# Performance work log

Hardware: AMD Instinct MI355X
Metric: run time of the kernel (lower is better)

The kernel has to match this reference:

```python
import jax, jax.numpy as jnp
import numpy as np

D_MODEL = 1024
NUM_HEADS = 16
D_K = D_MODEL // NUM_HEADS  # 64
B, S = 4, 1024


def setup_inputs() -> dict:
    key = jax.random.key(0)
    ks = jax.random.split(key, 8)
    scale = 1.0 / np.sqrt(D_MODEL)
    return {
        "query": jax.random.normal(ks[0], (B, S, D_MODEL), dtype=jnp.float32),
        "key": jax.random.normal(ks[1], (B, S, D_MODEL), dtype=jnp.float32),
        "value": jax.random.normal(ks[2], (B, S, D_MODEL), dtype=jnp.float32),
        "mask": jnp.ones((B, S, S), dtype=jnp.int32),
        # per-head projection weights, stacked: [H, d_model, d_k]
        "Wq": jax.random.normal(ks[3], (NUM_HEADS, D_MODEL, D_K), dtype=jnp.float32) * scale,
        "Wk": jax.random.normal(ks[4], (NUM_HEADS, D_MODEL, D_K), dtype=jnp.float32) * scale,
        "Wv": jax.random.normal(ks[5], (NUM_HEADS, D_MODEL, D_K), dtype=jnp.float32) * scale,
        # out projection: [H*d_v, d_model]
        "Wo": jax.random.normal(ks[6], (NUM_HEADS * D_K, D_MODEL), dtype=jnp.float32) * scale,
    }


def reference(query, key, value, mask, Wq, Wk, Wv, Wo):
    H, _, d_k = Wq.shape
    b, s, _ = query.shape
    inv_sqrt_dk = 1.0 / np.sqrt(d_k).astype(np.float32)
    # per-head projections (vectorized over heads): [H, B, S, d_k]
    q = jnp.einsum("bsd,hdk->hbsk", query, Wq)
    k = jnp.einsum("bsd,hdk->hbsk", key, Wk)
    v = jnp.einsum("bsd,hdk->hbsk", value, Wv)
    # raw scores before masking are what the torch module returns as q_key_dots
    scores = jnp.einsum("hbqk,hbmk->hbqm", q, k) * inv_sqrt_dk  # [H,B,Sq,Sk]
    masked = jnp.where(mask[None, :, :, :] == 0, -jnp.inf, scores)
    p_attn = jax.nn.softmax(masked, axis=-1)
    attn_out = jnp.einsum("hbqm,hbmk->hbqk", p_attn, v)  # [H,B,S,d_k]
    # concat heads along last dim in head order (matches torch.cat over h)
    concat = jnp.transpose(attn_out, (1, 2, 0, 3)).reshape(b, s, H * d_k)
    out = concat @ Wo  # [B,S,d_model]
    # torch returns (out, list of per-head masked scores); stack as [H,B,S,S]
    return out, masked
```

## Files before the change

### kernel.cpp

```cpp
#include <hip/hip_runtime.h>
#include <hip/hip_bf16.h>
#include <math.h>

typedef __attribute__((ext_vector_type(8))) short short8;
typedef __attribute__((ext_vector_type(4))) float f32x4;


static __device__ __forceinline__ unsigned short f2bf(float x) {
  union { float f; unsigned u; } v; v.f = x;
  unsigned r = v.u + 0x7fffu + ((v.u >> 16) & 1u);
  return (unsigned short)(r >> 16);
}

__global__ __launch_bounds__(256) void proj_kernel(
    const float* __restrict__ q_in, const float* __restrict__ k_in,
    const float* __restrict__ v_in, const float* __restrict__ Wq,
    const float* __restrict__ Wk, const float* __restrict__ Wv,
    unsigned short* __restrict__ qws, unsigned short* __restrict__ kws,
    unsigned short* __restrict__ vws) {
  __shared__ unsigned short As[64 * 72];
  __shared__ unsigned short Bs[64 * 72];
  const int tid = threadIdx.x;
  const int s0 = blockIdx.x * 64;
  const int h = blockIdx.y;
  const int b = blockIdx.z & 3;
  const int which = blockIdx.z >> 2;
  const float* X = which == 0 ? q_in : (which == 1 ? k_in : v_in);
  const float* W = which == 0 ? Wq : (which == 1 ? Wk : Wv);

  const int w = tid >> 6, lane = tid & 63, q16 = lane & 15, quad = lane >> 4;

  f32x4 acc[4];
  #pragma unroll
  for (int j = 0; j < 4; ++j) acc[j] = (f32x4)0.0f;

  for (int kt = 0; kt < 16; ++kt) {
    #pragma unroll
    for (int p = 0; p < 4; ++p) {
      int idx = tid + p * 256;
      int r = idx >> 4, c4 = idx & 15;
      const float4 v = *(const float4*)(X + (size_t)(b * 1024 + s0 + r) * 1024 + kt * 64 + c4 * 4);
      ushort4 u;
      u.x = f2bf(v.x); u.y = f2bf(v.y); u.z = f2bf(v.z); u.w = f2bf(v.w);
      *(ushort4*)&As[r * 72 + c4 * 4] = u;
    }
    #pragma unroll
    for (int p = 0; p < 16; ++p) {
      int dl = p * 4 + (tid >> 6);
      int n = tid & 63;
      float wv = W[(size_t)h * 65536 + (size_t)(kt * 64 + dl) * 64 + n];
      Bs[n * 72 + dl] = f2bf(wv);
    }
    __syncthreads();
    #pragma unroll
    for (int kk = 0; kk < 2; ++kk) {
      short8 a = *(const short8*)&As[(w * 16 + q16) * 72 + kk * 32 + quad * 8];
      #pragma unroll
      for (int j = 0; j < 4; ++j) {
        short8 bb = *(const short8*)&Bs[(j * 16 + q16) * 72 + kk * 32 + quad * 8];
        acc[j] = __builtin_amdgcn_mfma_f32_16x16x32_bf16(a, bb, acc[j], 0, 0, 0);
      }
    }
    __syncthreads();
  }

  const size_t bh = (size_t)(b * 16 + h);
  #pragma unroll
  for (int j = 0; j < 4; ++j) {
    #pragma unroll
    for (int r = 0; r < 4; ++r) {
      int sl = w * 16 + quad * 4 + r;
      int ko = j * 16 + q16;
      unsigned short val = f2bf(acc[j][r]);
      if (which == 2)
        vws[(bh * 64 + ko) * 1024 + (s0 + sl)] = val;
      else if (which == 1)
        kws[(bh * 1024 + (s0 + sl)) * 64 + ko] = val;
      else
        qws[(bh * 1024 + (s0 + sl)) * 64 + ko] = val;
    }
  }
}

__global__ __launch_bounds__(256) void attn_kernel(
    const unsigned short* __restrict__ qws, const unsigned short* __restrict__ kws,
    const unsigned short* __restrict__ vws, const int* __restrict__ mask,
    float* __restrict__ scores, unsigned short* __restrict__ cws) {
  __shared__ unsigned short Qs[64 * 72];
  __shared__ unsigned short Ks[64 * 72];
  __shared__ unsigned short Vts[64 * 72];
  __shared__ unsigned short Ps[64 * 72];
  const int tid = threadIdx.x;
  const int q0 = blockIdx.x * 64;
  const int h = blockIdx.y;
  const int b = blockIdx.z;
  const int w = tid >> 6, lane = tid & 63, q16 = lane & 15, quad = lane >> 4;
  const size_t bh = (size_t)(b * 16 + h);

  {
    const unsigned short* src = qws + (bh * 1024 + q0) * 64;
    #pragma unroll
    for (int p = 0; p < 2; ++p) {
      int idx = tid + p * 256, r = idx >> 3, c = idx & 7;
      *(uint4*)&Qs[r * 72 + c * 8] = *(const uint4*)(src + r * 64 + c * 8);
    }
  }

  f32x4 o[4];
  #pragma unroll
  for (int j = 0; j < 4; ++j) o[j] = (f32x4)0.0f;
  float m_run[4] = {-3.0e38f, -3.0e38f, -3.0e38f, -3.0e38f};
  float l_run[4] = {0.f, 0.f, 0.f, 0.f};

  for (int kt = 0; kt < 16; ++kt) {
    {
      const unsigned short* ksrc = kws + (bh * 1024 + (size_t)kt * 64) * 64;
      const unsigned short* vsrc = vws + bh * 64 * 1024 + kt * 64;
      #pragma unroll
      for (int p = 0; p < 2; ++p) {
        int idx = tid + p * 256, r = idx >> 3, c = idx & 7;
        *(uint4*)&Ks[r * 72 + c * 8] = *(const uint4*)(ksrc + r * 64 + c * 8);
        *(uint4*)&Vts[r * 72 + c * 8] = *(const uint4*)(vsrc + (size_t)r * 1024 + c * 8);
      }
    }
    __syncthreads();

    f32x4 sacc[4];
    #pragma unroll
    for (int j = 0; j < 4; ++j) sacc[j] = (f32x4)0.0f;
    #pragma unroll
    for (int kk = 0; kk < 2; ++kk) {
      short8 a = *(const short8*)&Qs[(w * 16 + q16) * 72 + kk * 32 + quad * 8];
      #pragma unroll
      for (int j = 0; j < 4; ++j) {
        short8 bb = *(const short8*)&Ks[(j * 16 + q16) * 72 + kk * 32 + quad * 8];
        sacc[j] = __builtin_amdgcn_mfma_f32_16x16x32_bf16(a, bb, sacc[j], 0, 0, 0);
      }
    }

    float rm[4] = {-3.0e38f, -3.0e38f, -3.0e38f, -3.0e38f};
    #pragma unroll
    for (int j = 0; j < 4; ++j) {
      #pragma unroll
      for (int r = 0; r < 4; ++r) {
        int ql = w * 16 + quad * 4 + r;
        int q = q0 + ql;
        int key = kt * 64 + j * 16 + q16;
        int mk = mask[((size_t)b * 1024 + q) * 1024 + key];
        float sv = sacc[j][r] * 0.125f;
        scores[(((size_t)h * 4 + b) * 1024 + q) * 1024 + key] = mk ? sv : -INFINITY;
        sv = mk ? sv : -3.0e38f;
        sacc[j][r] = sv;
        rm[r] = fmaxf(rm[r], sv);
      }
    }
    #pragma unroll
    for (int mM = 1; mM <= 8; mM <<= 1) {
      #pragma unroll
      for (int r = 0; r < 4; ++r) rm[r] = fmaxf(rm[r], __shfl_xor(rm[r], mM));
    }
    float rs[4];
    #pragma unroll
    for (int r = 0; r < 4; ++r) {
      float mnew = fmaxf(m_run[r], rm[r]);
      float alpha = __expf(m_run[r] - mnew);
      m_run[r] = mnew;
      l_run[r] *= alpha;
      #pragma unroll
      for (int j = 0; j < 4; ++j) o[j][r] *= alpha;
      rs[r] = 0.f;
    }
    #pragma unroll
    for (int j = 0; j < 4; ++j) {
      #pragma unroll
      for (int r = 0; r < 4; ++r) {
        float p = __expf(sacc[j][r] - m_run[r]);
        rs[r] += p;
        int ql = w * 16 + quad * 4 + r;
        Ps[ql * 72 + j * 16 + q16] = f2bf(p);
      }
    }
    #pragma unroll
    for (int mM = 1; mM <= 8; mM <<= 1) {
      #pragma unroll
      for (int r = 0; r < 4; ++r) rs[r] += __shfl_xor(rs[r], mM);
    }
    #pragma unroll
    for (int r = 0; r < 4; ++r) l_run[r] += rs[r];
    __syncthreads();

    #pragma unroll
    for (int kk = 0; kk < 2; ++kk) {
      short8 a = *(const short8*)&Ps[(w * 16 + q16) * 72 + kk * 32 + quad * 8];
      #pragma unroll
      for (int j = 0; j < 4; ++j) {
        short8 bb = *(const short8*)&Vts[(j * 16 + q16) * 72 + kk * 32 + quad * 8];
        o[j] = __builtin_amdgcn_mfma_f32_16x16x32_bf16(a, bb, o[j], 0, 0, 0);
      }
    }
    __syncthreads();
  }

  float inv[4];
  #pragma unroll
  for (int r = 0; r < 4; ++r) inv[r] = 1.0f / l_run[r];
  #pragma unroll
  for (int j = 0; j < 4; ++j) {
    #pragma unroll
    for (int r = 0; r < 4; ++r) {
      int ql = w * 16 + quad * 4 + r;
      int d = j * 16 + q16;
      cws[((size_t)(b * 1024 + q0 + ql)) * 1024 + h * 64 + d] = f2bf(o[j][r] * inv[r]);
    }
  }
}

__global__ __launch_bounds__(256) void outproj_kernel(
    const unsigned short* __restrict__ cws, const float* __restrict__ Wo,
    float* __restrict__ out) {
  __shared__ unsigned short As[64 * 72];
  __shared__ unsigned short Bs[64 * 72];
  const int tid = threadIdx.x;
  const int m0 = blockIdx.x * 64;
  const int n0 = blockIdx.y * 64;
  const int w = tid >> 6, lane = tid & 63, q16 = lane & 15, quad = lane >> 4;
  f32x4 acc[4];
  #pragma unroll
  for (int j = 0; j < 4; ++j) acc[j] = (f32x4)0.0f;

  for (int kt = 0; kt < 16; ++kt) {
    #pragma unroll
    for (int p = 0; p < 2; ++p) {
      int idx = tid + p * 256, r = idx >> 3, c = idx & 7;
      *(uint4*)&As[r * 72 + c * 8] = *(const uint4*)(cws + (size_t)(m0 + r) * 1024 + kt * 64 + c * 8);
    }
    #pragma unroll
    for (int p = 0; p < 16; ++p) {
      int kr = p * 4 + (tid >> 6);
      int n = tid & 63;
      Bs[n * 72 + kr] = f2bf(Wo[(size_t)(kt * 64 + kr) * 1024 + n0 + n]);
    }
    __syncthreads();
    #pragma unroll
    for (int kk = 0; kk < 2; ++kk) {
      short8 a = *(const short8*)&As[(w * 16 + q16) * 72 + kk * 32 + quad * 8];
      #pragma unroll
      for (int j = 0; j < 4; ++j) {
        short8 bb = *(const short8*)&Bs[(j * 16 + q16) * 72 + kk * 32 + quad * 8];
        acc[j] = __builtin_amdgcn_mfma_f32_16x16x32_bf16(a, bb, acc[j], 0, 0, 0);
      }
    }
    __syncthreads();
  }
  #pragma unroll
  for (int j = 0; j < 4; ++j) {
    #pragma unroll
    for (int r = 0; r < 4; ++r) {
      out[(size_t)(m0 + w * 16 + quad * 4 + r) * 1024 + n0 + j * 16 + q16] = acc[j][r];
    }
  }
}

extern "C" void kernel_launch(void* const* d_in, const int* in_sizes, int n_in,
                              void* d_out, int out_size, void* d_ws, size_t ws_size,
                              hipStream_t stream) {
  (void)in_sizes; (void)n_in; (void)out_size; (void)ws_size;
  const float* q_in = (const float*)d_in[0];
  const float* k_in = (const float*)d_in[1];
  const float* v_in = (const float*)d_in[2];
  const int* mask   = (const int*)d_in[3];
  const float* Wq   = (const float*)d_in[4];
  const float* Wk   = (const float*)d_in[5];
  const float* Wv   = (const float*)d_in[6];
  const float* Wo   = (const float*)d_in[7];

  float* out = (float*)d_out;
  float* scores = out + (size_t)4 * 1024 * 1024;

  unsigned short* qws = (unsigned short*)d_ws;
  unsigned short* kws = qws + (size_t)4 * 16 * 1024 * 64;
  unsigned short* vws = kws + (size_t)4 * 16 * 1024 * 64;
  unsigned short* cws = vws + (size_t)4 * 16 * 1024 * 64;

  proj_kernel<<<dim3(16, 16, 12), 256, 0, stream>>>(q_in, k_in, v_in, Wq, Wk, Wv, qws, kws, vws);
  attn_kernel<<<dim3(16, 16, 4), 256, 0, stream>>>(qws, kws, vws, mask, scores, cws);
  outproj_kernel<<<dim3(64, 16), 256, 0, stream>>>(cws, Wo, out);
}
```

Measured before the change: 542.7 us.

## Pre-convert inputs and weights to bf16, enlarge GEMM tiles, prefetch K/V in attention

```diff
diff --git a/kernel.cpp b/kernel.cpp
--- a/kernel.cpp
+++ b/kernel.cpp
@@ -12,72 +12,142 @@
   return (unsigned short)(r >> 16);
 }
 
+__global__ __launch_bounds__(256) void convert_x_kernel(
+    const float* __restrict__ q, const float* __restrict__ k,
+    const float* __restrict__ v, unsigned short* __restrict__ xq,
+    unsigned short* __restrict__ xk, unsigned short* __restrict__ xv) {
+  const float* src = blockIdx.y == 0 ? q : (blockIdx.y == 1 ? k : v);
+  unsigned short* dst = blockIdx.y == 0 ? xq : (blockIdx.y == 1 ? xk : xv);
+  size_t i = ((size_t)blockIdx.x * 256 + threadIdx.x) * 4;
+  float4 f = *(const float4*)(src + i);
+  ushort4 u;
+  u.x = f2bf(f.x); u.y = f2bf(f.y); u.z = f2bf(f.z); u.w = f2bf(f.w);
+  *(ushort4*)(dst + i) = u;
+}
+
+__global__ __launch_bounds__(256) void prep_w_kernel(
+    const float* __restrict__ Wq, const float* __restrict__ Wk,
+    const float* __restrict__ Wv, const float* __restrict__ Wo,
+    unsigned short* __restrict__ Wtq, unsigned short* __restrict__ Wtk,
+    unsigned short* __restrict__ Wtv, unsigned short* __restrict__ Wto) {
+  __shared__ unsigned short Lt[64 * 72];
+  const int tid = threadIdx.x;
+  const int which = blockIdx.y;
+  const int kt = blockIdx.x & 15, hn = blockIdx.x >> 4;
+  const float* src;
+  unsigned short* dst;
+  size_t sbase; int sld;
+  if (which < 3) {
+    src = which == 0 ? Wq : (which == 1 ? Wk : Wv);
+    dst = which == 0 ? Wtq : (which == 1 ? Wtk : Wtv);
+    sbase = (size_t)hn * 65536 + (size_t)kt * 4096;
+    sld = 64;
+  } else {
+    src = Wo; dst = Wto;
+    sbase = (size_t)kt * 65536 + (size_t)hn * 64;
+    sld = 1024;
+  }
+  const size_t dbase = (size_t)hn * 65536 + (size_t)kt * 64;
+
+  #pragma unroll
+  for (int p = 0; p < 4; ++p) {
+    int idx = tid + p * 256;
+    int r = idx >> 4, c = (idx & 15) * 4;
+    float4 f = *(const float4*)(src + sbase + (size_t)r * sld + c);
+    Lt[(c + 0) * 72 + r] = f2bf(f.x);
+    Lt[(c + 1) * 72 + r] = f2bf(f.y);
+    Lt[(c + 2) * 72 + r] = f2bf(f.z);
+    Lt[(c + 3) * 72 + r] = f2bf(f.w);
+  }
+  __syncthreads();
+  #pragma unroll
+  for (int p = 0; p < 2; ++p) {
+    int idx = tid + p * 256;
+    int r = idx >> 3, c = (idx & 7) * 8;
+    *(uint4*)(dst + dbase + (size_t)r * 1024 + c) = *(const uint4*)&Lt[r * 72 + c];
+  }
+}
+
 __global__ __launch_bounds__(256) void proj_kernel(
-    const float* __restrict__ q_in, const float* __restrict__ k_in,
-    const float* __restrict__ v_in, const float* __restrict__ Wq,
-    const float* __restrict__ Wk, const float* __restrict__ Wv,
+    const unsigned short* __restrict__ xq, const unsigned short* __restrict__ xk,
+    const unsigned short* __restrict__ xv, const unsigned short* __restrict__ Wtq,
+    const unsigned short* __restrict__ Wtk, const unsigned short* __restrict__ Wtv,
     unsigned short* __restrict__ qws, unsigned short* __restrict__ kws,
     unsigned short* __restrict__ vws) {
-  __shared__ unsigned short As[64 * 72];
+  __shared__ unsigned short As[128 * 72];
   __shared__ unsigned short Bs[64 * 72];
   const int tid = threadIdx.x;
-  const int s0 = blockIdx.x * 64;
+  const int m0 = blockIdx.x * 128;
   const int h = blockIdx.y;
-  const int b = blockIdx.z & 3;
-  const int which = blockIdx.z >> 2;
-  const float* X = which == 0 ? q_in : (which == 1 ? k_in : v_in);
-  const float* W = which == 0 ? Wq : (which == 1 ? Wk : Wv);
-
+  const int which = blockIdx.z;
+  const unsigned short* X = which == 0 ? xq : (which == 1 ? xk : xv);
+  const unsigned short* Wt = (which == 0 ? Wtq : (which == 1 ? Wtk : Wtv)) + (size_t)h * 65536;
   const int w = tid >> 6, lane = tid & 63, q16 = lane & 15, quad = lane >> 4;
 
-  f32x4 acc[4];
-  #pragma unroll
-  for (int j = 0; j < 4; ++j) acc[j] = (f32x4)0.0f;
+  f32x4 acc[2][4];
+  #pragma unroll
+  for (int g = 0; g < 2; ++g)
+    #pragma unroll
+    for (int j = 0; j < 4; ++j) acc[g][j] = (f32x4)0.0f;
 
   for (int kt = 0; kt < 16; ++kt) {
     #pragma unroll
     for (int p = 0; p < 4; ++p) {
-      int idx = tid + p * 256;
-      int r = idx >> 4, c4 = idx & 15;
-      const float4 v = *(const float4*)(X + (size_t)(b * 1024 + s0 + r) * 1024 + kt * 64 + c4 * 4);
-      ushort4 u;
-      u.x = f2bf(v.x); u.y = f2bf(v.y); u.z = f2bf(v.z); u.w = f2bf(v.w);
-      *(ushort4*)&As[r * 72 + c4 * 4] = u;
-    }
-    #pragma unroll
-    for (int p = 0; p < 16; ++p) {
-      int dl = p * 4 + (tid >> 6);
-      int n = tid & 63;
-      float wv = W[(size_t)h * 65536 + (size_t)(kt * 64 + dl) * 64 + n];
-      Bs[n * 72 + dl] = f2bf(wv);
+      int idx = tid + p * 256, r = idx >> 3, c = (idx & 7) * 8;
+      *(uint4*)&As[r * 72 + c] = *(const uint4*)(X + (size_t)(m0 + r) * 1024 + kt * 64 + c);
+    }
+    #pragma unroll
+    for (int p = 0; p < 2; ++p) {
+      int idx = tid + p * 256, r = idx >> 3, c = (idx & 7) * 8;
+      *(uint4*)&Bs[r * 72 + c] = *(const uint4*)(Wt + (size_t)r * 1024 + kt * 64 + c);
     }
     __syncthreads();
     #pragma unroll
     for (int kk = 0; kk < 2; ++kk) {
-      short8 a = *(const short8*)&As[(w * 16 + q16) * 72 + kk * 32 + quad * 8];
+      short8 a0 = *(const short8*)&As[(w * 32 + q16) * 72 + kk * 32 + quad * 8];
+      short8 a1 = *(const short8*)&As[(w * 32 + 16 + q16) * 72 + kk * 32 + quad * 8];
       #pragma unroll
       for (int j = 0; j < 4; ++j) {
         short8 bb = *(const short8*)&Bs[(j * 16 + q16) * 72 + kk * 32 + quad * 8];
-        acc[j] = __builtin_amdgcn_mfma_f32_16x16x32_bf16(a, bb, acc[j], 0, 0, 0);
-      }
-    }
-    __syncthreads();
-  }
-
+        acc[0][j] = __builtin_amdgcn_mfma_f32_16x16x32_bf16(a0, bb, acc[0][j], 0, 0, 0);
+        acc[1][j] = __builtin_amdgcn_mfma_f32_16x16x32_bf16(a1, bb, acc[1][j], 0, 0, 0);
+      }
+    }
+    __syncthreads();
+  }
+
+  const int b = m0 >> 10, s0 = m0 & 1023;
   const size_t bh = (size_t)(b * 16 + h);
-  #pragma unroll
-  for (int j = 0; j < 4; ++j) {
-    #pragma unroll
-    for (int r = 0; r < 4; ++r) {
-      int sl = w * 16 + quad * 4 + r;
-      int ko = j * 16 + q16;
-      unsigned short val = f2bf(acc[j][r]);
-      if (which == 2)
-        vws[(bh * 64 + ko) * 1024 + (s0 + sl)] = val;
-      else if (which == 1)
-        kws[(bh * 1024 + (s0 + sl)) * 64 + ko] = val;
-      else
-        qws[(bh * 1024 + (s0 + sl)) * 64 + ko] = val;
+  if (which == 2) {
+    unsigned short* Lt = As;
+    #pragma unroll
+    for (int g = 0; g < 2; ++g)
+      #pragma unroll
+      for (int j = 0; j < 4; ++j)
+        #pragma unroll
+        for (int r = 0; r < 4; ++r)
+          Lt[(j * 16 + q16) * 136 + (w * 32 + g * 16 + quad * 4 + r)] = f2bf(acc[g][j][r]);
+    __syncthreads();
+    #pragma unroll
+    for (int p = 0; p < 4; ++p) {
+      int idx = tid + p * 256, r = idx >> 4, c = (idx & 15) * 8;
+      *(uint4*)(vws + (bh * 64 + r) * 1024 + s0 + c) = *(const uint4*)&Lt[r * 136 + c];
+    }
+  } else {
+    unsigned short* Lt = As;
+    #pragma unroll
+    for (int g = 0; g < 2; ++g)
+      #pragma unroll
+      for (int j = 0; j < 4; ++j)
+        #pragma unroll
+        for (int r = 0; r < 4; ++r)
+          Lt[(w * 32 + g * 16 + quad * 4 + r) * 72 + j * 16 + q16] = f2bf(acc[g][j][r]);
+    __syncthreads();
+    unsigned short* outp = which == 1 ? kws : qws;
+    #pragma unroll
+    for (int p = 0; p < 4; ++p) {
+      int idx = tid + p * 256, r = idx >> 3, c = (idx & 7) * 8;
+      *(uint4*)(outp + (bh * 1024 + s0 + r) * 64 + c) = *(const uint4*)&Lt[r * 72 + c];
     }
   }
 }
@@ -86,7 +156,6 @@
     const unsigned short* __restrict__ qws, const unsigned short* __restrict__ kws,
     const unsigned short* __restrict__ vws, const int* __restrict__ mask,
     float* __restrict__ scores, unsigned short* __restrict__ cws) {
-  __shared__ unsigned short Qs[64 * 72];
   __shared__ unsigned short Ks[64 * 72];
   __shared__ unsigned short Vts[64 * 72];
   __shared__ unsigned short Ps[64 * 72];
@@ -97,12 +166,20 @@
   const int w = tid >> 6, lane = tid & 63, q16 = lane & 15, quad = lane >> 4;
   const size_t bh = (size_t)(b * 16 + h);
 
+  short8 aq[2];
+  #pragma unroll
+  for (int kk = 0; kk < 2; ++kk)
+    aq[kk] = *(const short8*)(qws + (bh * 1024 + q0 + w * 16 + q16) * 64 + kk * 32 + quad * 8);
+
+  uint4 kr[2], vr[2];
+  const unsigned short* kbase = kws + bh * 1024 * 64;
+  const unsigned short* vbase = vws + bh * 64 * 1024;
   {
-    const unsigned short* src = qws + (bh * 1024 + q0) * 64;
     #pragma unroll
     for (int p = 0; p < 2; ++p) {
-      int idx = tid + p * 256, r = idx >> 3, c = idx & 7;
-      *(uint4*)&Qs[r * 72 + c * 8] = *(const uint4*)(src + r * 64 + c * 8);
+      int idx = tid + p * 256, r = idx >> 3, c = (idx & 7) * 8;
+      kr[p] = *(const uint4*)(kbase + (size_t)r * 64 + c);
+      vr[p] = *(const uint4*)(vbase + (size_t)r * 1024 + c);
     }
   }
 
@@ -113,28 +190,39 @@
   float l_run[4] = {0.f, 0.f, 0.f, 0.f};
 
   for (int kt = 0; kt < 16; ++kt) {
-    {
-      const unsigned short* ksrc = kws + (bh * 1024 + (size_t)kt * 64) * 64;
-      const unsigned short* vsrc = vws + bh * 64 * 1024 + kt * 64;
+    #pragma unroll
+    for (int p = 0; p < 2; ++p) {
+      int idx = tid + p * 256, r = idx >> 3, c = (idx & 7) * 8;
+      *(uint4*)&Ks[r * 72 + c] = kr[p];
+      *(uint4*)&Vts[r * 72 + c] = vr[p];
+    }
+    __syncthreads();
+
+    int mk[4][4];
+    #pragma unroll
+    for (int j = 0; j < 4; ++j)
+      #pragma unroll
+      for (int r = 0; r < 4; ++r)
+        mk[j][r] = mask[((size_t)b * 1024 + q0 + w * 16 + quad * 4 + r) * 1024 + kt * 64 + j * 16 + q16];
+
+    if (kt < 15) {
       #pragma unroll
       for (int p = 0; p < 2; ++p) {
-        int idx = tid + p * 256, r = idx >> 3, c = idx & 7;
-        *(uint4*)&Ks[r * 72 + c * 8] = *(const uint4*)(ksrc + r * 64 + c * 8);
-        *(uint4*)&Vts[r * 72 + c * 8] = *(const uint4*)(vsrc + (size_t)r * 1024 + c * 8);
-      }
-    }
-    __syncthreads();
+        int idx = tid + p * 256, r = idx >> 3, c = (idx & 7) * 8;
+        kr[p] = *(const uint4*)(kbase + (size_t)(kt + 1) * 64 * 64 + (size_t)r * 64 + c);
+        vr[p] = *(const uint4*)(vbase + (size_t)(kt + 1) * 64 + (size_t)r * 1024 + c);
+      }
+    }
 
     f32x4 sacc[4];
     #pragma unroll
     for (int j = 0; j < 4; ++j) sacc[j] = (f32x4)0.0f;
     #pragma unroll
     for (int kk = 0; kk < 2; ++kk) {
-      short8 a = *(const short8*)&Qs[(w * 16 + q16) * 72 + kk * 32 + quad * 8];
       #pragma unroll
       for (int j = 0; j < 4; ++j) {
         short8 bb = *(const short8*)&Ks[(j * 16 + q16) * 72 + kk * 32 + quad * 8];
-        sacc[j] = __builtin_amdgcn_mfma_f32_16x16x32_bf16(a, bb, sacc[j], 0, 0, 0);
+        sacc[j] = __builtin_amdgcn_mfma_f32_16x16x32_bf16(aq[kk], bb, sacc[j], 0, 0, 0);
       }
     }
 
@@ -143,13 +231,11 @@
     for (int j = 0; j < 4; ++j) {
       #pragma unroll
       for (int r = 0; r < 4; ++r) {
-        int ql = w * 16 + quad * 4 + r;
-        int q = q0 + ql;
+        int q = q0 + w * 16 + quad * 4 + r;
         int key = kt * 64 + j * 16 + q16;
-        int mk = mask[((size_t)b * 1024 + q) * 1024 + key];
         float sv = sacc[j][r] * 0.125f;
-        scores[(((size_t)h * 4 + b) * 1024 + q) * 1024 + key] = mk ? sv : -INFINITY;
-        sv = mk ? sv : -3.0e38f;
+        scores[(((size_t)h * 4 + b) * 1024 + q) * 1024 + key] = mk[j][r] ? sv : -INFINITY;
+        sv = mk[j][r] ? sv : -3.0e38f;
         sacc[j][r] = sv;
         rm[r] = fmaxf(rm[r], sv);
       }
@@ -176,8 +262,7 @@
       for (int r = 0; r < 4; ++r) {
         float p = __expf(sacc[j][r] - m_run[r]);
         rs[r] += p;
-        int ql = w * 16 + quad * 4 + r;
-        Ps[ql * 72 + j * 16 + q16] = f2bf(p);
+        Ps[(w * 16 + quad * 4 + r) * 72 + j * 16 + q16] = f2bf(p);
       }
     }
     #pragma unroll
@@ -187,7 +272,6 @@
     }
     #pragma unroll
     for (int r = 0; r < 4; ++r) l_run[r] += rs[r];
-    __syncthreads();
 
     #pragma unroll
     for (int kk = 0; kk < 2; ++kk) {
@@ -209,56 +293,60 @@
     #pragma unroll
     for (int r = 0; r < 4; ++r) {
       int ql = w * 16 + quad * 4 + r;
-      int d = j * 16 + q16;
-      cws[((size_t)(b * 1024 + q0 + ql)) * 1024 + h * 64 + d] = f2bf(o[j][r] * inv[r]);
+      cws[((size_t)(b * 1024 + q0 + ql)) * 1024 + h * 64 + j * 16 + q16] = f2bf(o[j][r] * inv[r]);
     }
   }
 }
 
 __global__ __launch_bounds__(256) void outproj_kernel(
-    const unsigned short* __restrict__ cws, const float* __restrict__ Wo,
+    const unsigned short* __restrict__ cws, const unsigned short* __restrict__ Wto,
     float* __restrict__ out) {
-  __shared__ unsigned short As[64 * 72];
+  __shared__ unsigned short As[128 * 72];
   __shared__ unsigned short Bs[64 * 72];
   const int tid = threadIdx.x;
-  const int m0 = blockIdx.x * 64;
+  const int m0 = blockIdx.x * 128;
   const int n0 = blockIdx.y * 64;
   const int w = tid >> 6, lane = tid & 63, q16 = lane & 15, quad = lane >> 4;
-  f32x4 acc[4];
-  #pragma unroll
-  for (int j = 0; j < 4; ++j) acc[j] = (f32x4)0.0f;
+  const unsigned short* Bsrc = Wto + (size_t)n0 * 1024;
+
+  f32x4 acc[2][4];
+  #pragma unroll
+  for (int g = 0; g < 2; ++g)
+    #pragma unroll
+    for (int j = 0; j < 4; ++j) acc[g][j] = (f32x4)0.0f;
 
   for (int kt = 0; kt < 16; ++kt) {
     #pragma unroll
+    for (int p = 0; p < 4; ++p) {
+      int idx = tid + p * 256, r = idx >> 3, c = (idx & 7) * 8;
+      *(uint4*)&As[r * 72 + c] = *(const uint4*)(cws + (size_t)(m0 + r) * 1024 + kt * 64 + c);
+    }
+    #pragma unroll
     for (int p = 0; p < 2; ++p) {
-      int idx = tid + p * 256, r = idx >> 3, c = idx & 7;
-      *(uint4*)&As[r * 72 + c * 8] = *(const uint4*)(cws + (size_t)(m0 + r) * 1024 + kt * 64 + c * 8);
-    }
-    #pragma unroll
-    for (int p = 0; p < 16; ++p) {
-      int kr = p * 4 + (tid >> 6);
-      int n = tid & 63;
-      Bs[n * 72 + kr] = f2bf(Wo[(size_t)(kt * 64 + kr) * 1024 + n0 + n]);
+      int idx = tid + p * 256, r = idx >> 3, c = (idx & 7) * 8;
+      *(uint4*)&Bs[r * 72 + c] = *(const uint4*)(Bsrc + (size_t)r * 1024 + kt * 64 + c);
     }
     __syncthreads();
     #pragma unroll
     for (int kk = 0; kk < 2; ++kk) {
-      short8 a = *(const short8*)&As[(w * 16 + q16) * 72 + kk * 32 + quad * 8];
+      short8 a0 = *(const short8*)&As[(w * 32 + q16) * 72 + kk * 32 + quad * 8];
+      short8 a1 = *(const short8*)&As[(w * 32 + 16 + q16) * 72 + kk * 32 + quad * 8];
       #pragma unroll
       for (int j = 0; j < 4; ++j) {
         short8 bb = *(const short8*)&Bs[(j * 16 + q16) * 72 + kk * 32 + quad * 8];
-        acc[j] = __builtin_amdgcn_mfma_f32_16x16x32_bf16(a, bb, acc[j], 0, 0, 0);
-      }
-    }
-    __syncthreads();
-  }
-  #pragma unroll
-  for (int j = 0; j < 4; ++j) {
-    #pragma unroll
-    for (int r = 0; r < 4; ++r) {
-      out[(size_t)(m0 + w * 16 + quad * 4 + r) * 1024 + n0 + j * 16 + q16] = acc[j][r];
-    }
-  }
+        acc[0][j] = __builtin_amdgcn_mfma_f32_16x16x32_bf16(a0, bb, acc[0][j], 0, 0, 0);
+        acc[1][j] = __builtin_amdgcn_mfma_f32_16x16x32_bf16(a1, bb, acc[1][j], 0, 0, 0);
+      }
+    }
+    __syncthreads();
+  }
+  #pragma unroll
+  for (int g = 0; g < 2; ++g)
+    #pragma unroll
+    for (int j = 0; j < 4; ++j)
+      #pragma unroll
+      for (int r = 0; r < 4; ++r)
+        out[(size_t)(m0 + w * 32 + g * 16 + quad * 4 + r) * 1024 + n0 + j * 16 + q16] = acc[g][j][r];
 }
 
 extern "C" void kernel_launch(void* const* d_in, const int* in_sizes, int n_in,
@@ -277,12 +365,23 @@
   float* out = (float*)d_out;
   float* scores = out + (size_t)4 * 1024 * 1024;
 
-  unsigned short* qws = (unsigned short*)d_ws;
-  unsigned short* kws = qws + (size_t)4 * 16 * 1024 * 64;
-  unsigned short* vws = kws + (size_t)4 * 16 * 1024 * 64;
-  unsigned short* cws = vws + (size_t)4 * 16 * 1024 * 64;
-
-  proj_kernel<<<dim3(16, 16, 12), 256, 0, stream>>>(q_in, k_in, v_in, Wq, Wk, Wv, qws, kws, vws);
+  const size_t NX = (size_t)4 * 1024 * 1024;
+  const size_t NW = (size_t)1024 * 1024;
+  unsigned short* xq  = (unsigned short*)d_ws;
+  unsigned short* xk  = xq + NX;
+  unsigned short* xv  = xk + NX;
+  unsigned short* Wtq = xv + NX;
+  unsigned short* Wtk = Wtq + NW;
+  unsigned short* Wtv = Wtk + NW;
+  unsigned short* Wto = Wtv + NW;
+  unsigned short* qws = Wto + NW;
+  unsigned short* kws = qws + NX;
+  unsigned short* vws = kws + NX;
+  unsigned short* cws = vws + NX;
+
+  convert_x_kernel<<<dim3(4096, 3), 256, 0, stream>>>(q_in, k_in, v_in, xq, xk, xv);
+  prep_w_kernel<<<dim3(256, 4), 256, 0, stream>>>(Wq, Wk, Wv, Wo, Wtq, Wtk, Wtv, Wto);
+  proj_kernel<<<dim3(32, 16, 3), 256, 0, stream>>>(xq, xk, xv, Wtq, Wtk, Wtv, qws, kws, vws);
   attn_kernel<<<dim3(16, 16, 4), 256, 0, stream>>>(qws, kws, vws, mask, scores, cws);
-  outproj_kernel<<<dim3(64, 16), 256, 0, stream>>>(cws, Wo, out);
-}
+  outproj_kernel<<<dim3(32, 16), 256, 0, stream>>>(cws, Wto, out);
+}
```

Result: slower. 616.4 us (+13.6%).
